# Kernel tuning notes

Measured on AMD Instinct MI355X. Metric: run time of the kernel, lower is better.

Reference implementation:

```python
import jax, jax.numpy as jnp
import numpy as np

EPS = 1e-05


def setup_inputs() -> dict:
    key = jax.random.key(0)
    k1, k2 = jax.random.split(key)
    shape = (4, 1, 192, 192, 192)  # [B, C=1, D, H, W]
    y_pred = jax.random.normal(k1, shape, dtype=jnp.float32)
    y_true = jax.random.normal(k2, shape, dtype=jnp.float32)
    return {"y_pred": y_pred, "y_true": y_true}


def reference(y_pred, y_true):
    # ones-filter conv is exactly a global sum over channel+spatial dims.
    Ii, Ji = y_true, y_pred
    axes = tuple(range(1, Ii.ndim))  # sum over C, D, H, W -> per-batch scalar
    win_size = jnp.asarray(np.prod(Ii.shape[2:]), dtype=Ii.dtype)

    I_sum = jnp.sum(Ii, axis=axes)
    J_sum = jnp.sum(Ji, axis=axes)
    I2_sum = jnp.sum(Ii * Ii, axis=axes)
    J2_sum = jnp.sum(Ji * Ji, axis=axes)
    IJ_sum = jnp.sum(Ii * Ji, axis=axes)

    u_I = I_sum / win_size
    u_J = J_sum / win_size

    cross = IJ_sum - u_J * I_sum - u_I * J_sum + u_I * u_J * win_size
    I_var = I2_sum - 2 * u_I * I_sum + u_I * u_I * win_size
    J_var = J2_sum - 2 * u_J * J_sum + u_J * u_J * win_size

    cc = cross / (jnp.sqrt(I_var) * jnp.sqrt(J_var) + EPS)  # [B]
    # original: reshape to [B, 1] then mean over dim 1 -> [B]
    return cc
```

## Files before the change

kernel.cpp:

```cpp
#include <hip/hip_runtime.h>
#include <math.h>

#define EPS 1e-05

static constexpr int BLOCK  = 256;
static constexpr int BPB    = 256;
static constexpr int KPT    = 27;
static constexpr int NBATCH = 4;
static constexpr long long NPB = 192LL * 192LL * 192LL;

typedef float v4f __attribute__((ext_vector_type(4)));

__device__ __forceinline__ double wave_reduce(double v) {
    #pragma unroll
    for (int off = 32; off > 0; off >>= 1)
        v += __shfl_down(v, off, 64);
    return v;
}

__global__ __launch_bounds__(BLOCK) void ncc_partial(
    const float* __restrict__ y_pred, const float* __restrict__ y_true,
    double* __restrict__ part)
{
    const int b  = blockIdx.y;
    const int bx = blockIdx.x;
    const v4f* __restrict__ I4 = (const v4f*)(y_true + (long long)b * NPB);
    const v4f* __restrict__ J4 = (const v4f*)(y_pred + (long long)b * NPB);

    const unsigned base = (unsigned)bx * (BLOCK * KPT) + threadIdx.x;

    double sI = 0.0, sJ = 0.0, sI2 = 0.0, sJ2 = 0.0, sIJ = 0.0;
    #pragma unroll
    for (int k = 0; k < KPT; ++k) {
        v4f a = __builtin_nontemporal_load(I4 + base + k * BLOCK);
        v4f c = __builtin_nontemporal_load(J4 + base + k * BLOCK);
        float gI  = (a.x + a.y) + (a.z + a.w);
        float gJ  = (c.x + c.y) + (c.z + c.w);
        float gI2 = fmaf(a.x, a.x, fmaf(a.y, a.y, fmaf(a.z, a.z, a.w * a.w)));
        float gJ2 = fmaf(c.x, c.x, fmaf(c.y, c.y, fmaf(c.z, c.z, c.w * c.w)));
        float gIJ = fmaf(a.x, c.x, fmaf(a.y, c.y, fmaf(a.z, c.z, a.w * c.w)));
        sI  += (double)gI;
        sJ  += (double)gJ;
        sI2 += (double)gI2;
        sJ2 += (double)gJ2;
        sIJ += (double)gIJ;
    }

    sI  = wave_reduce(sI);
    sJ  = wave_reduce(sJ);
    sI2 = wave_reduce(sI2);
    sJ2 = wave_reduce(sJ2);
    sIJ = wave_reduce(sIJ);

    __shared__ double lds[BLOCK / 64][5];
    const int wave = threadIdx.x >> 6;
    const int lane = threadIdx.x & 63;
    if (lane == 0) {
        lds[wave][0] = sI;  lds[wave][1] = sJ;
        lds[wave][2] = sI2; lds[wave][3] = sJ2;
        lds[wave][4] = sIJ;
    }
    __syncthreads();
    if (threadIdx.x == 0) {
        double* p = part + ((long long)b * BPB + bx) * 5;
        #pragma unroll
        for (int k = 0; k < 5; ++k)
            p[k] = ((lds[0][k] + lds[1][k]) + (lds[2][k] + lds[3][k]));
    }
}

__global__ __launch_bounds__(BLOCK) void ncc_final(
    const double* __restrict__ part, float* __restrict__ out)
{
    const int b = blockIdx.x;
    const double* p = part + ((long long)b * BPB + threadIdx.x) * 5;
    double s[5];
    #pragma unroll
    for (int k = 0; k < 5; ++k) s[k] = p[k];
    #pragma unroll
    for (int k = 0; k < 5; ++k) s[k] = wave_reduce(s[k]);

    __shared__ double lds[BLOCK / 64][5];
    const int wave = threadIdx.x >> 6;
    const int lane = threadIdx.x & 63;
    if (lane == 0) {
        #pragma unroll
        for (int k = 0; k < 5; ++k) lds[wave][k] = s[k];
    }
    __syncthreads();
    if (threadIdx.x == 0) {
        double I_sum  = (lds[0][0] + lds[1][0]) + (lds[2][0] + lds[3][0]);
        double J_sum  = (lds[0][1] + lds[1][1]) + (lds[2][1] + lds[3][1]);
        double I2_sum = (lds[0][2] + lds[1][2]) + (lds[2][2] + lds[3][2]);
        double J2_sum = (lds[0][3] + lds[1][3]) + (lds[2][3] + lds[3][3]);
        double IJ_sum = (lds[0][4] + lds[1][4]) + (lds[2][4] + lds[3][4]);

        const double win = (double)NPB;
        const double u_I = I_sum / win;
        const double u_J = J_sum / win;
        const double cross = IJ_sum - u_J * I_sum - u_I * J_sum + u_I * u_J * win;
        const double I_var = I2_sum - 2.0 * u_I * I_sum + u_I * u_I * win;
        const double J_var = J2_sum - 2.0 * u_J * J_sum + u_J * u_J * win;
        const double cc = cross / (sqrt(I_var) * sqrt(J_var) + EPS);
        out[b] = (float)cc;
    }
}

extern "C" void kernel_launch(void* const* d_in, const int* in_sizes, int n_in,
                              void* d_out, int out_size, void* d_ws, size_t ws_size,
                              hipStream_t stream) {
    const float* y_pred = (const float*)d_in[0];
    const float* y_true = (const float*)d_in[1];
    float* out = (float*)d_out;
    double* part = (double*)d_ws;

    dim3 grid1(BPB, NBATCH);
    ncc_partial<<<grid1, BLOCK, 0, stream>>>(y_pred, y_true, part);
    ncc_final<<<NBATCH, BLOCK, 0, stream>>>(part, out);
}
```

Baseline: 215.4 us.

## Use more blocks with fp32 vector accumulators in NCC partial reduction

Result: no change. 215.7 us (+0.1%).

```diff
diff --git a/kernel.cpp b/kernel.cpp
--- a/kernel.cpp
+++ b/kernel.cpp
@@ -4,8 +4,8 @@
 #define EPS 1e-05
 
 static constexpr int BLOCK  = 256;
-static constexpr int BPB    = 256;
-static constexpr int KPT    = 27;
+static constexpr int BPB    = 768;
+static constexpr int KPT    = 9;
 static constexpr int NBATCH = 4;
 static constexpr long long NPB = 192LL * 192LL * 192LL;
 
@@ -18,7 +18,7 @@
     return v;
 }
 
-__global__ __launch_bounds__(BLOCK) void ncc_partial(
+__global__ __launch_bounds__(BLOCK, 4) void ncc_partial(
     const float* __restrict__ y_pred, const float* __restrict__ y_true,
     double* __restrict__ part)
 {
@@ -29,22 +29,28 @@
 
     const unsigned base = (unsigned)bx * (BLOCK * KPT) + threadIdx.x;
 
-    double sI = 0.0, sJ = 0.0, sI2 = 0.0, sJ2 = 0.0, sIJ = 0.0;
+    v4f vI  = {0.f, 0.f, 0.f, 0.f};
+    v4f vJ  = {0.f, 0.f, 0.f, 0.f};
+    v4f vI2 = {0.f, 0.f, 0.f, 0.f};
+    v4f vJ2 = {0.f, 0.f, 0.f, 0.f};
+    v4f vIJ = {0.f, 0.f, 0.f, 0.f};
+
     #pragma unroll
     for (int k = 0; k < KPT; ++k) {
         v4f a = __builtin_nontemporal_load(I4 + base + k * BLOCK);
         v4f c = __builtin_nontemporal_load(J4 + base + k * BLOCK);
-        float gI  = (a.x + a.y) + (a.z + a.w);
-        float gJ  = (c.x + c.y) + (c.z + c.w);
-        float gI2 = fmaf(a.x, a.x, fmaf(a.y, a.y, fmaf(a.z, a.z, a.w * a.w)));
-        float gJ2 = fmaf(c.x, c.x, fmaf(c.y, c.y, fmaf(c.z, c.z, c.w * c.w)));
-        float gIJ = fmaf(a.x, c.x, fmaf(a.y, c.y, fmaf(a.z, c.z, a.w * c.w)));
-        sI  += (double)gI;
-        sJ  += (double)gJ;
-        sI2 += (double)gI2;
-        sJ2 += (double)gJ2;
-        sIJ += (double)gIJ;
+        vI  += a;
+        vJ  += c;
+        vI2 += a * a;
+        vJ2 += c * c;
+        vIJ += a * c;
     }
+
+    double sI  = ((double)vI.x  + (double)vI.y)  + ((double)vI.z  + (double)vI.w);
+    double sJ  = ((double)vJ.x  + (double)vJ.y)  + ((double)vJ.z  + (double)vJ.w);
+    double sI2 = ((double)vI2.x + (double)vI2.y) + ((double)vI2.z + (double)vI2.w);
+    double sJ2 = ((double)vJ2.x + (double)vJ2.y) + ((double)vJ2.z + (double)vJ2.w);
+    double sIJ = ((double)vIJ.x + (double)vIJ.y) + ((double)vIJ.z + (double)vIJ.w);
 
     sI  = wave_reduce(sI);
     sJ  = wave_reduce(sJ);
@@ -73,10 +79,13 @@
     const double* __restrict__ part, float* __restrict__ out)
 {
     const int b = blockIdx.x;
-    const double* p = part + ((long long)b * BPB + threadIdx.x) * 5;
-    double s[5];
+    double s[5] = {0.0, 0.0, 0.0, 0.0, 0.0};
     #pragma unroll
-    for (int k = 0; k < 5; ++k) s[k] = p[k];
+    for (int j = 0; j < BPB / BLOCK; ++j) {
+        const double* p = part + ((long long)b * BPB + j * BLOCK + threadIdx.x) * 5;
+        #pragma unroll
+        for (int k = 0; k < 5; ++k) s[k] += p[k];
+    }
     #pragma unroll
     for (int k = 0; k < 5; ++k) s[k] = wave_reduce(s[k]);
 
```
